# Optimization experiments

Hardware: AMD Instinct MI355X
Metric: run time of the kernel (lower is better)

The kernel has to match this reference:

```python
import jax, jax.numpy as jnp
import numpy as np

DIM = 512
HEADS = 8
WIN = 64
HIDDEN = 2048
EPS = 1e-5


def layernorm(x, g, b):
    mu = jnp.mean(x, axis=-1, keepdims=True)
    var = jnp.var(x, axis=-1, keepdims=True)
    return (x - mu) * jax.lax.rsqrt(var + EPS) * g + b


def setup_inputs() -> dict:
    key = jax.random.key(0)
    ks = jax.random.split(key, 10)
    s = lambda fan_in: 1.0 / np.sqrt(fan_in)
    return {
        "x": jax.random.normal(ks[0], (8, 4096, DIM), dtype=jnp.float32),
        "ln1_g": jnp.ones((DIM,), jnp.float32),
        "ln1_b": jnp.zeros((DIM,), jnp.float32),
        "qkv_w": jax.random.normal(ks[1], (DIM, 3 * DIM), jnp.float32) * s(DIM),
        "qkv_b": jnp.zeros((3 * DIM,), jnp.float32),
        "proj_w": jax.random.normal(ks[2], (DIM, DIM), jnp.float32) * s(DIM),
        "proj_b": jnp.zeros((DIM,), jnp.float32),
        "ln2_g": jnp.ones((DIM,), jnp.float32),
        "ln2_b": jnp.zeros((DIM,), jnp.float32),
        "fc1_w": jax.random.normal(ks[3], (DIM, HIDDEN), jnp.float32) * s(DIM),
        "fc1_b": jnp.zeros((HIDDEN,), jnp.float32),
        "fc2_w": jax.random.normal(ks[4], (HIDDEN, DIM), jnp.float32) * s(HIDDEN),
        "fc2_b": jnp.zeros((DIM,), jnp.float32),
    }


def reference(x, ln1_g, ln1_b, qkv_w, qkv_b, proj_w, proj_b, ln2_g, ln2_b,
              fc1_w, fc1_b, fc2_w, fc2_b):
    B, N, C = x.shape
    hd = C // HEADS
    scale = hd ** -0.5

    # --- W-MSA (shift_size forced to 0, attn_mask None) ---
    h = layernorm(x, ln1_g, ln1_b)
    hw = h.reshape(B * (N // WIN), WIN, C)
    qkv = hw @ qkv_w + qkv_b
    qkv = qkv.reshape(-1, WIN, 3, HEADS, hd)
    q = qkv[:, :, 0] * scale
    k = qkv[:, :, 1]
    v = qkv[:, :, 2]
    attn = jnp.einsum('bqhd,bkhd->bhqk', q, k)
    attn = jax.nn.softmax(attn, axis=-1)
    o = jnp.einsum('bhqk,bkhd->bqhd', attn, v).reshape(-1, WIN, C)
    o = o @ proj_w + proj_b
    x = x + o.reshape(B, N, C)

    # --- MLP (GELU exact, dropout=0) ---
    h2 = layernorm(x, ln2_g, ln2_b)
    h2 = jax.nn.gelu(h2 @ fc1_w + fc1_b, approximate=False)
    x = x + (h2 @ fc2_w + fc2_b)
    return x
```

## Files before the change

### kernel.cpp

```cpp
#include <hip/hip_runtime.h>
#include <hip/hip_bf16.h>
#include <cstdint>

typedef unsigned short U16;
typedef float f32x4 __attribute__((ext_vector_type(4)));
typedef __bf16 bf16x8 __attribute__((ext_vector_type(8)));

#define DEVINL __device__ __forceinline__

DEVINL U16 f2bf(float f) {
    unsigned u = __float_as_uint(f);
    return (U16)((u + 0x7FFFu + ((u >> 16) & 1u)) >> 16);
}
DEVINL float bf2f(U16 s) { return __uint_as_float(((unsigned)s) << 16); }

DEVINL void gld16(const void* g, void* l) {
    __builtin_amdgcn_global_load_lds(
        (const __attribute__((address_space(1))) void*)g,
        (__attribute__((address_space(3))) void*)l, 16, 0, 0);
}

#define MFMA_BF16 __builtin_amdgcn_mfma_f32_16x16x32_bf16

__global__ __launch_bounds__(256) void tcast_kernel(const float* __restrict__ w,
                                                    U16* __restrict__ wt, int K, int N) {
    __shared__ float tile[32][33];
    int n0 = blockIdx.x * 32, k0 = blockIdx.y * 32;
    int tx = threadIdx.x, ty = threadIdx.y;
#pragma unroll
    for (int i = 0; i < 32; i += 8) tile[ty + i][tx] = w[(size_t)(k0 + ty + i) * N + (n0 + tx)];
    __syncthreads();
#pragma unroll
    for (int i = 0; i < 32; i += 8) wt[(size_t)(n0 + ty + i) * K + (k0 + tx)] = f2bf(tile[tx][ty + i]);
}

__global__ __launch_bounds__(256) void ln_kernel(const float* __restrict__ x,
                                                 const float* __restrict__ g,
                                                 const float* __restrict__ b,
                                                 U16* __restrict__ out) {
    int lane = threadIdx.x & 63;
    size_t row = (size_t)blockIdx.x * 4 + (threadIdx.x >> 6);
    const float4* xr = (const float4*)(x + row * 512);
    float4 v0 = xr[lane], v1 = xr[lane + 64];
    float s = (v0.x + v0.y) + (v0.z + v0.w) + (v1.x + v1.y) + (v1.z + v1.w);
    float sq = (v0.x * v0.x + v0.y * v0.y + v0.z * v0.z + v0.w * v0.w) +
               (v1.x * v1.x + v1.y * v1.y + v1.z * v1.z + v1.w * v1.w);
#pragma unroll
    for (int m = 1; m < 64; m <<= 1) { s += __shfl_xor(s, m); sq += __shfl_xor(sq, m); }
    float mu = s * (1.f / 512.f);
    float var = sq * (1.f / 512.f) - mu * mu;
    float rs = rsqrtf(var + 1e-5f);
    const float4* g4 = (const float4*)g;
    const float4* b4 = (const float4*)b;
    float4 gv = g4[lane], bv = b4[lane];
    ushort4 o;
    o.x = f2bf((v0.x - mu) * rs * gv.x + bv.x);
    o.y = f2bf((v0.y - mu) * rs * gv.y + bv.y);
    o.z = f2bf((v0.z - mu) * rs * gv.z + bv.z);
    o.w = f2bf((v0.w - mu) * rs * gv.w + bv.w);
    ((ushort4*)(out + row * 512))[lane] = o;
    gv = g4[lane + 64]; bv = b4[lane + 64];
    o.x = f2bf((v1.x - mu) * rs * gv.x + bv.x);
    o.y = f2bf((v1.y - mu) * rs * gv.y + bv.y);
    o.z = f2bf((v1.z - mu) * rs * gv.z + bv.z);
    o.w = f2bf((v1.w - mu) * rs * gv.w + bv.w);
    ((ushort4*)(out + row * 512))[lane + 64] = o;
}

template <int EPI, int K>
__global__ __launch_bounds__(512, 1) void gemm_rt(const U16* __restrict__ A,
                                                  const U16* __restrict__ Bt,
                                                  const float* __restrict__ bias,
                                                  const float* __restrict__ resid,
                                                  U16* __restrict__ outb,
                                                  float* __restrict__ outf,
                                                  int M, int N, int gridN) {
    __shared__ __align__(16) U16 smem[65536];

    const int tid = threadIdx.x;
    const int lane = tid & 63, wv = tid >> 6;
    const int lo = lane & 15, hi = lane >> 4;
    const int wm = wv >> 2, wn = wv & 3;

    const int nwg = gridDim.x, bid = blockIdx.x;
    const int swzb = (bid & 7) * (nwg >> 3) + (bid >> 3);
    const int bn = swzb % gridN, bm = swzb / gridN;

    const int sr = tid >> 2;
    const int lc = (tid & 3) ^ ((sr >> 1) & 3);
    const U16* gA0 = A + (size_t)(bm * 256 + sr) * K + lc * 8;
    const U16* gA1 = gA0 + (size_t)128 * K;
    const U16* gB0 = Bt + (size_t)(bn * 256 + sr) * K + lc * 8;
    const U16* gB1 = gB0 + (size_t)128 * K;

#define STAGE_A(t2)                                                   \
    do {                                                              \
        U16* _l = smem + ((t2) & 3) * 16384 + tid * 8;                \
        gld16(gA0 + (t2) * 32, _l);                                   \
        gld16(gA1 + (t2) * 32, _l + 4096);                            \
    } while (0)
#define STAGE_B(t2)                                                   \
    do {                                                              \
        U16* _l = smem + ((t2) & 3) * 16384 + 8192 + tid * 8;         \
        gld16(gB0 + (t2) * 32, _l);                                   \
        gld16(gB1 + (t2) * 32, _l + 4096);                            \
    } while (0)

    const int ck = (hi ^ ((lo >> 1) & 3)) << 3;
    const int aoff = (wm * 128 + lo) * 32 + ck;
    const int boff = 8192 + (wn * 64 + lo) * 32 + ck;

    f32x4 acc[8][4] = {};

    constexpr int NT = K >> 5;
    static_assert(NT >= 16 && (NT % 16) == 0, "K must be a multiple of 512");

    STAGE_A(0); STAGE_B(0);
    STAGE_A(1); STAGE_B(1);

#define ITER(t)                                                                 \
    do {                                                                        \
        if ((t) + 1 < NT) {                                                     \
            asm volatile("s_waitcnt vmcnt(4)" ::: "memory");                    \
        } else {                                                                \
            asm volatile("s_waitcnt vmcnt(0)" ::: "memory");                    \
        }                                                                       \
        __builtin_amdgcn_s_barrier();                                           \
        {                                                                       \
            const int _cb = ((t) & 3) * 16384;                                  \
            const U16* _Ab = smem + _cb + aoff;                                 \
            const U16* _Bb = smem + _cb + boff;                                 \
               \
            if ((t) + 2 < NT) STAGE_A((t) + 2);                                 \
            bf16x8 af[4], bg[4];                                                \
            _Pragma("unroll") for (int i = 0; i < 4; ++i)                       \
                af[i] = *(const bf16x8*)(_Ab + i * 512);                        \
            _Pragma("unroll") for (int j = 0; j < 4; ++j)                       \
                bg[j] = *(const bf16x8*)(_Bb + j * 512);                        \
            __builtin_amdgcn_s_setprio(1);                                      \
            _Pragma("unroll") for (int i = 0; i < 4; ++i)                       \
                _Pragma("unroll") for (int j = 0; j < 4; ++j)                   \
                    acc[i][j] = MFMA_BF16(af[i], bg[j], acc[i][j], 0, 0, 0);    \
            __builtin_amdgcn_s_setprio(0);                                      \
                              \
            if ((t) + 2 < NT) STAGE_B((t) + 2);                                 \
            bf16x8 af2[4];                                                      \
            _Pragma("unroll") for (int i = 0; i < 4; ++i)                       \
                af2[i] = *(const bf16x8*)(_Ab + (i + 4) * 512);                 \
            __builtin_amdgcn_s_setprio(1);                                      \
            _Pragma("unroll") for (int i = 0; i < 4; ++i)                       \
                _Pragma("unroll") for (int j = 0; j < 4; ++j)                   \
                    acc[4 + i][j] = MFMA_BF16(af2[i], bg[j], acc[4 + i][j], 0, 0, 0); \
            __builtin_amdgcn_s_setprio(0);                                      \
        }                                                                       \
    } while (0)

#pragma unroll
    for (int t0 = 0; t0 < NT; t0 += 16) {
#pragma unroll
        for (int tt = 0; tt < 16; ++tt) ITER(t0 + tt);
    }

    const int row0 = bm * 256 + wm * 128 + hi * 4;
    const int col0 = bn * 256 + wn * 64 + lo;
    float bc[4];
#pragma unroll
    for (int j = 0; j < 4; ++j) bc[j] = bias[col0 + j * 16];

    if (EPI == 1) {
#pragma unroll
        for (int i = 0; i < 8; ++i)
#pragma unroll
            for (int r = 0; r < 4; ++r) {
                const size_t rowb = (size_t)(row0 + i * 16 + r) * N;
#pragma unroll
                for (int j = 0; j < 4; ++j) {
                    const size_t idx = rowb + col0 + j * 16;
                    outf[idx] = acc[i][j][r] + bc[j] + resid[idx];
                }
            }
    } else {
#pragma unroll
        for (int i = 0; i < 8; ++i)
#pragma unroll
            for (int j = 0; j < 4; ++j)
#pragma unroll
                for (int r = 0; r < 4; ++r) {
                    float v = acc[i][j][r] + bc[j];
                    if (EPI == 2) {
                        float u = v * (0.7978845608028654f + 0.0356774081f * v * v);
                        v = v / (1.f + __expf(-2.f * u));
                    }
                    outb[(size_t)(row0 + i * 16 + r) * N + col0 + j * 16] = f2bf(v);
                }
    }
#undef ITER
#undef STAGE_A
#undef STAGE_B
}

__global__ __launch_bounds__(256) void attn_kernel(const U16* __restrict__ qkv,
                                                   U16* __restrict__ o) {
    const int blk = blockIdx.x;
    const int w = blk >> 3, h = blk & 7;
    const int tid = threadIdx.x;
    const int lane = tid & 63, wv = tid >> 6;
    const int lo = lane & 15, hi = lane >> 4;

    __shared__ __align__(16) U16 Qs[64][72];
    __shared__ __align__(16) U16 Ks[64][72];
    __shared__ __align__(16) U16 Vt[64][72];
    __shared__ __align__(16) U16 Ps[4][16][72];

    {
        const int r = tid >> 2;
        const int c0 = (tid & 3) << 4;
        const U16* p = qkv + (size_t)(w * 64 + r) * 1536 + h * 64 + c0;
        *(bf16x8*)&Ks[r][c0] = *(const bf16x8*)(p + 512);
        *(bf16x8*)&Ks[r][c0 + 8] = *(const bf16x8*)(p + 520);
        const U16* pv = p + 1024;
#pragma unroll
        for (int i = 0; i < 16; i++) Vt[c0 + i][r] = pv[i];
#pragma unroll
        for (int i = 0; i < 16; i++) Qs[r][c0 + i] = f2bf(bf2f(p[i]) * 0.125f);
    }
    __syncthreads();

    const int rb = wv * 16;
    f32x4 s[4] = {};
#pragma unroll
    for (int dc = 0; dc < 64; dc += 32) {
        bf16x8 a = *(const bf16x8*)&Qs[rb + lo][dc + hi * 8];
#pragma unroll
        for (int jb = 0; jb < 4; jb++) {
            bf16x8 bfr = *(const bf16x8*)&Ks[jb * 16 + lo][dc + hi * 8];
            s[jb] = MFMA_BF16(a, bfr, s[jb], 0, 0, 0);
        }
    }
#pragma unroll
    for (int r = 0; r < 4; r++) {
        float m = fmaxf(fmaxf(s[0][r], s[1][r]), fmaxf(s[2][r], s[3][r]));
#pragma unroll
        for (int msk = 1; msk < 16; msk <<= 1) m = fmaxf(m, __shfl_xor(m, msk));
        float e[4], sum = 0.f;
#pragma unroll
        for (int jb = 0; jb < 4; jb++) { e[jb] = __expf(s[jb][r] - m); sum += e[jb]; }
#pragma unroll
        for (int msk = 1; msk < 16; msk <<= 1) sum += __shfl_xor(sum, msk);
        float inv = 1.f / sum;
#pragma unroll
        for (int jb = 0; jb < 4; jb++) Ps[wv][hi * 4 + r][jb * 16 + lo] = f2bf(e[jb] * inv);
    }
    __syncthreads();

    f32x4 oa[4] = {};
#pragma unroll
    for (int jc = 0; jc < 64; jc += 32) {
        bf16x8 a = *(const bf16x8*)&Ps[wv][lo][jc + hi * 8];
#pragma unroll
        for (int db = 0; db < 4; db++) {
            bf16x8 bfr = *(const bf16x8*)&Vt[db * 16 + lo][jc + hi * 8];
            oa[db] = MFMA_BF16(a, bfr, oa[db], 0, 0, 0);
        }
    }
#pragma unroll
    for (int db = 0; db < 4; db++)
#pragma unroll
        for (int r = 0; r < 4; r++)
            o[(size_t)(w * 64 + rb + hi * 4 + r) * 512 + h * 64 + db * 16 + lo] = f2bf(oa[db][r]);
}

extern "C" void kernel_launch(void* const* d_in, const int* in_sizes, int n_in,
                              void* d_out, int out_size, void* d_ws, size_t ws_size,
                              hipStream_t stream) {
    const float* x = (const float*)d_in[0];
    const float* ln1_g = (const float*)d_in[1];
    const float* ln1_b = (const float*)d_in[2];
    const float* qkv_w = (const float*)d_in[3];
    const float* qkv_b = (const float*)d_in[4];
    const float* proj_w = (const float*)d_in[5];
    const float* proj_b = (const float*)d_in[6];
    const float* ln2_g = (const float*)d_in[7];
    const float* ln2_b = (const float*)d_in[8];
    const float* fc1_w = (const float*)d_in[9];
    const float* fc1_b = (const float*)d_in[10];
    const float* fc2_w = (const float*)d_in[11];
    const float* fc2_b = (const float*)d_in[12];
    float* out = (float*)d_out;

    char* ws = (char*)d_ws;
    U16* hbuf = (U16*)ws;
    U16* big = (U16*)(ws + 33554432);
    U16* wt_qkv = (U16*)(ws + 33554432 + 134217728);
    U16* wt_proj = wt_qkv + 1536 * 512;
    U16* wt_fc1 = wt_proj + 512 * 512;
    U16* wt_fc2 = wt_fc1 + 2048 * 512;

    dim3 tb(32, 8);
    tcast_kernel<<<dim3(1536 / 32, 512 / 32), tb, 0, stream>>>(qkv_w, wt_qkv, 512, 1536);
    tcast_kernel<<<dim3(512 / 32, 512 / 32), tb, 0, stream>>>(proj_w, wt_proj, 512, 512);
    tcast_kernel<<<dim3(2048 / 32, 512 / 32), tb, 0, stream>>>(fc1_w, wt_fc1, 512, 2048);
    tcast_kernel<<<dim3(512 / 32, 2048 / 32), tb, 0, stream>>>(fc2_w, wt_fc2, 2048, 512);

    ln_kernel<<<8192, 256, 0, stream>>>(x, ln1_g, ln1_b, hbuf);
    gemm_rt<0, 512><<<768, 512, 0, stream>>>(hbuf, wt_qkv, qkv_b, nullptr, big, nullptr, 32768, 1536, 6);
    attn_kernel<<<4096, 256, 0, stream>>>(big, hbuf);
    gemm_rt<1, 512><<<256, 512, 0, stream>>>(hbuf, wt_proj, proj_b, x, nullptr, out, 32768, 512, 2);
    ln_kernel<<<8192, 256, 0, stream>>>(out, ln2_g, ln2_b, hbuf);
    gemm_rt<2, 512><<<1024, 512, 0, stream>>>(hbuf, wt_fc1, fc1_b, nullptr, big, nullptr, 32768, 2048, 8);
    gemm_rt<1, 2048><<<256, 512, 0, stream>>>(big, wt_fc2, fc2_b, out, nullptr, out, 32768, 512, 2);
}
```

Baseline: 363.2 us.

## Restructure GEMM mainloop to BK=64 double-buffer with quarter-tile staged prefetch

The GEMM main loop moves from a 4-stage ring of K=32 tiles to a 2-stage double buffer of K=64 tiles, with an 8-way XOR swizzle on the LDS layout. Each K-step is split into four MFMA phases, and each phase is interleaved with a quarter-tile global->LDS prefetch and extra barriers, in the style of an 8-wave ping-pong schedule. The goal is fewer waitcnt/barrier rounds per unit of K and better overlap of loads with MFMA work. In exchange it adds more barriers per step and a more fragile ordering of LDS reuse. The prefetch distances also differ: A is loaded one step ahead and B two steps ahead into a two-slot buffer.

New measurement: 352.5 us. 2.9% less time.

```diff
diff --git a/kernel.cpp b/kernel.cpp
--- a/kernel.cpp
+++ b/kernel.cpp
@@ -86,80 +86,117 @@
     const int swzb = (bid & 7) * (nwg >> 3) + (bid >> 3);
     const int bn = swzb % gridN, bm = swzb / gridN;
 
-    const int sr = tid >> 2;
-    const int lc = (tid & 3) ^ ((sr >> 1) & 3);
-    const U16* gA0 = A + (size_t)(bm * 256 + sr) * K + lc * 8;
-    const U16* gA1 = gA0 + (size_t)128 * K;
-    const U16* gB0 = Bt + (size_t)(bn * 256 + sr) * K + lc * 8;
-    const U16* gB1 = gB0 + (size_t)128 * K;
-
-#define STAGE_A(t2)                                                   \
-    do {                                                              \
-        U16* _l = smem + ((t2) & 3) * 16384 + tid * 8;                \
-        gld16(gA0 + (t2) * 32, _l);                                   \
-        gld16(gA1 + (t2) * 32, _l + 4096);                            \
-    } while (0)
-#define STAGE_B(t2)                                                   \
-    do {                                                              \
-        U16* _l = smem + ((t2) & 3) * 16384 + 8192 + tid * 8;         \
-        gld16(gB0 + (t2) * 32, _l);                                   \
-        gld16(gB1 + (t2) * 32, _l + 4096);                            \
-    } while (0)
-
-    const int ck = (hi ^ ((lo >> 1) & 3)) << 3;
-    const int aoff = (wm * 128 + lo) * 32 + ck;
-    const int boff = 8192 + (wn * 64 + lo) * 32 + ck;
+    const int sr2 = tid >> 3;
+    const int lc8 = (tid & 7) ^ (sr2 & 7);
+    const U16* gAh = A + (size_t)(bm * 256 + sr2) * K + lc8 * 8;
+    const U16* gBh = Bt + (size_t)(bn * 256 + sr2) * K + lc8 * 8;
+
+#define SA0(t)                                                              \
+    do { U16* _l = smem + ((t) & 1) * 32768 + tid * 8;                      \
+         gld16(gAh + (t) * 64, _l);                                         \
+         gld16(gAh + (size_t)64 * K + (t) * 64, _l + 4096); } while (0)
+#define SA1(t)                                                              \
+    do { U16* _l = smem + ((t) & 1) * 32768 + 8192 + tid * 8;               \
+         gld16(gAh + (size_t)128 * K + (t) * 64, _l);                       \
+         gld16(gAh + (size_t)192 * K + (t) * 64, _l + 4096); } while (0)
+#define SB0(t)                                                              \
+    do { U16* _l = smem + ((t) & 1) * 32768 + 16384 + tid * 8;              \
+         gld16(gBh + (t) * 64, _l);                                         \
+         gld16(gBh + (size_t)64 * K + (t) * 64, _l + 4096); } while (0)
+#define SB1(t)                                                              \
+    do { U16* _l = smem + ((t) & 1) * 32768 + 24576 + tid * 8;              \
+         gld16(gBh + (size_t)128 * K + (t) * 64, _l);                       \
+         gld16(gBh + (size_t)192 * K + (t) * 64, _l + 4096); } while (0)
+
+    const int ck0 = (hi ^ (lo & 7)) << 3;
+    const int ck1 = ((4 | hi) ^ (lo & 7)) << 3;
+    const int abase = wm * 8192 + lo * 64;
+    const int bbase = 16384 + (wn >> 1) * 8192 + ((wn & 1) * 64 + lo) * 64;
 
     f32x4 acc[8][4] = {};
 
-    constexpr int NT = K >> 5;
-    static_assert(NT >= 16 && (NT % 16) == 0, "K must be a multiple of 512");
-
-    STAGE_A(0); STAGE_B(0);
-    STAGE_A(1); STAGE_B(1);
-
-#define ITER(t)                                                                 \
+    constexpr int NT = K >> 6;
+    static_assert(NT >= 4 && (NT % 4) == 0, "K must be a multiple of 256");
+
+    SA0(0); SA1(0); SB0(0); SB1(0);
+    SB0(1); SB1(1);
+    asm volatile("s_waitcnt vmcnt(4)" ::: "memory");
+    __builtin_amdgcn_s_barrier();
+
+#define ITER(s)                                                                 \
     do {                                                                        \
-        if ((t) + 1 < NT) {                                                     \
+        const int _cb = ((s) & 1) * 32768;                                      \
+        const U16* _Ab = smem + _cb + abase;                                    \
+        const U16* _Bb = smem + _cb + bbase;                                    \
+        bf16x8 af[4][2], bg[4][2], af2[4][2];                                   \
+              \
+        _Pragma("unroll") for (int i = 0; i < 4; ++i) {                         \
+            af[i][0] = *(const bf16x8*)(_Ab + i * 1024 + ck0);                  \
+            af[i][1] = *(const bf16x8*)(_Ab + i * 1024 + ck1);                  \
+        }                                                                       \
+        _Pragma("unroll") for (int j = 0; j < 2; ++j) {                         \
+            bg[j][0] = *(const bf16x8*)(_Bb + j * 1024 + ck0);                  \
+            bg[j][1] = *(const bf16x8*)(_Bb + j * 1024 + ck1);                  \
+        }                                                                       \
+        if ((s) + 1 < NT) SA0((s) + 1);                                         \
+        __builtin_amdgcn_s_barrier();                                           \
+        __builtin_amdgcn_s_setprio(1);                                          \
+        _Pragma("unroll") for (int i = 0; i < 4; ++i)                           \
+            _Pragma("unroll") for (int j = 0; j < 2; ++j) {                     \
+                acc[i][j] = MFMA_BF16(af[i][0], bg[j][0], acc[i][j], 0, 0, 0);  \
+                acc[i][j] = MFMA_BF16(af[i][1], bg[j][1], acc[i][j], 0, 0, 0);  \
+            }                                                                   \
+        __builtin_amdgcn_s_setprio(0);                                          \
+        __builtin_amdgcn_s_barrier();                                           \
+                    \
+        _Pragma("unroll") for (int j = 2; j < 4; ++j) {                         \
+            bg[j][0] = *(const bf16x8*)(_Bb + j * 1024 + ck0);                  \
+            bg[j][1] = *(const bf16x8*)(_Bb + j * 1024 + ck1);                  \
+        }                                                                       \
+        if ((s) + 1 < NT) SA1((s) + 1);                                         \
+        __builtin_amdgcn_s_barrier();                                           \
+        __builtin_amdgcn_s_setprio(1);                                          \
+        _Pragma("unroll") for (int i = 0; i < 4; ++i)                           \
+            _Pragma("unroll") for (int j = 2; j < 4; ++j) {                     \
+                acc[i][j] = MFMA_BF16(af[i][0], bg[j][0], acc[i][j], 0, 0, 0);  \
+                acc[i][j] = MFMA_BF16(af[i][1], bg[j][1], acc[i][j], 0, 0, 0);  \
+            }                                                                   \
+        __builtin_amdgcn_s_setprio(0);                                          \
+        __builtin_amdgcn_s_barrier();                                           \
+                     \
+        _Pragma("unroll") for (int i = 0; i < 4; ++i) {                         \
+            af2[i][0] = *(const bf16x8*)(_Ab + 4096 + i * 1024 + ck0);          \
+            af2[i][1] = *(const bf16x8*)(_Ab + 4096 + i * 1024 + ck1);          \
+        }                                                                       \
+        if ((s) + 2 < NT) SB0((s) + 2);                                         \
+        __builtin_amdgcn_s_barrier();                                           \
+        __builtin_amdgcn_s_setprio(1);                                          \
+        _Pragma("unroll") for (int i = 0; i < 4; ++i)                           \
+            _Pragma("unroll") for (int j = 0; j < 2; ++j) {                     \
+                acc[4 + i][j] = MFMA_BF16(af2[i][0], bg[j][0], acc[4 + i][j], 0, 0, 0); \
+                acc[4 + i][j] = MFMA_BF16(af2[i][1], bg[j][1], acc[4 + i][j], 0, 0, 0); \
+            }                                                                   \
+        __builtin_amdgcn_s_setprio(0);                                          \
+        __builtin_amdgcn_s_barrier();                                           \
+                              \
+        if ((s) + 2 < NT) SB1((s) + 2);                                         \
+        __builtin_amdgcn_s_setprio(1);                                          \
+        _Pragma("unroll") for (int i = 0; i < 4; ++i)                           \
+            _Pragma("unroll") for (int j = 2; j < 4; ++j) {                     \
+                acc[4 + i][j] = MFMA_BF16(af2[i][0], bg[j][0], acc[4 + i][j], 0, 0, 0); \
+                acc[4 + i][j] = MFMA_BF16(af2[i][1], bg[j][1], acc[4 + i][j], 0, 0, 0); \
+            }                                                                   \
+        __builtin_amdgcn_s_setprio(0);                                          \
+        if ((s) + 2 < NT) {                                                     \
             asm volatile("s_waitcnt vmcnt(4)" ::: "memory");                    \
         } else {                                                                \
             asm volatile("s_waitcnt vmcnt(0)" ::: "memory");                    \
         }                                                                       \
         __builtin_amdgcn_s_barrier();                                           \
-        {                                                                       \
-            const int _cb = ((t) & 3) * 16384;                                  \
-            const U16* _Ab = smem + _cb + aoff;                                 \
-            const U16* _Bb = smem + _cb + boff;                                 \
-               \
-            if ((t) + 2 < NT) STAGE_A((t) + 2);                                 \
-            bf16x8 af[4], bg[4];                                                \
-            _Pragma("unroll") for (int i = 0; i < 4; ++i)                       \
-                af[i] = *(const bf16x8*)(_Ab + i * 512);                        \
-            _Pragma("unroll") for (int j = 0; j < 4; ++j)                       \
-                bg[j] = *(const bf16x8*)(_Bb + j * 512);                        \
-            __builtin_amdgcn_s_setprio(1);                                      \
-            _Pragma("unroll") for (int i = 0; i < 4; ++i)                       \
-                _Pragma("unroll") for (int j = 0; j < 4; ++j)                   \
-                    acc[i][j] = MFMA_BF16(af[i], bg[j], acc[i][j], 0, 0, 0);    \
-            __builtin_amdgcn_s_setprio(0);                                      \
-                              \
-            if ((t) + 2 < NT) STAGE_B((t) + 2);                                 \
-            bf16x8 af2[4];                                                      \
-            _Pragma("unroll") for (int i = 0; i < 4; ++i)                       \
-                af2[i] = *(const bf16x8*)(_Ab + (i + 4) * 512);                 \
-            __builtin_amdgcn_s_setprio(1);                                      \
-            _Pragma("unroll") for (int i = 0; i < 4; ++i)                       \
-                _Pragma("unroll") for (int j = 0; j < 4; ++j)                   \
-                    acc[4 + i][j] = MFMA_BF16(af2[i], bg[j], acc[4 + i][j], 0, 0, 0); \
-            __builtin_amdgcn_s_setprio(0);                                      \
-        }                                                                       \
     } while (0)
 
 #pragma unroll
-    for (int t0 = 0; t0 < NT; t0 += 16) {
-#pragma unroll
-        for (int tt = 0; tt < 16; ++tt) ITER(t0 + tt);
-    }
+    for (int s = 0; s < NT; ++s) ITER(s);
 
     const int row0 = bm * 256 + wm * 128 + hi * 4;
     const int col0 = bn * 256 + wn * 64 + lo;
@@ -195,8 +232,10 @@
                 }
     }
 #undef ITER
-#undef STAGE_A
-#undef STAGE_B
+#undef SA0
+#undef SA1
+#undef SB0
+#undef SB1
 }
 
 __global__ __launch_bounds__(256) void attn_kernel(const U16* __restrict__ qkv,
```
